# Optimization experiments

Hardware: AMD Instinct MI355X
Metric: run time of the kernel (lower is better)

## Reference

```python
import jax, jax.numpy as jnp
import numpy as np

N = 50000
E = 800000
IN_DIM, HID, LAT, DEC_HID = 256, 256, 128, 512


def _glorot(key, shape):
    fan_in, fan_out = shape
    lim = np.sqrt(6.0 / (fan_in + fan_out))
    return jax.random.uniform(key, shape, jnp.float32, -lim, lim)


def setup_inputs() -> dict:
    key = jax.random.key(0)
    ks = jax.random.split(key, 10)
    x = jax.random.normal(ks[0], (N, IN_DIM), jnp.float32)
    edge_index = jax.random.randint(ks[1], (2, E), 0, N, dtype=jnp.int64)
    return {
        "x": x,
        "edge_index": edge_index,
        "W1": _glorot(ks[2], (IN_DIM, HID)), "b1": jnp.zeros((HID,), jnp.float32),
        "W2": _glorot(ks[3], (HID, LAT)), "b2": jnp.zeros((LAT,), jnp.float32),
        "Wd1": _glorot(ks[4], (LAT, DEC_HID)), "bd1": jnp.zeros((DEC_HID,), jnp.float32),
        "Wd2": _glorot(ks[5], (DEC_HID, IN_DIM)), "bd2": jnp.zeros((IN_DIM,), jnp.float32),
    }


def _gcn_layer(x, src, dst, W, b, num_nodes):
    # linear transform
    xt = x @ W + b                      # [N, out]
    # scatter-mean aggregation over incoming edges (PyG aggr='mean')
    msg = xt[src]                       # [E, out] gather of source features
    summed = jax.ops.segment_sum(msg, dst, num_segments=num_nodes)
    cnt = jax.ops.segment_sum(jnp.ones((src.shape[0],), xt.dtype), dst,
                              num_segments=num_nodes)
    mean = summed / jnp.maximum(cnt, 1.0)[:, None]   # 0 for isolated nodes
    # relu + residual
    return jax.nn.relu(mean) + xt


def reference(x, edge_index, W1, b1, W2, b2, Wd1, bd1, Wd2, bd2):
    src, dst = edge_index[0], edge_index[1]
    h = _gcn_layer(x, src, dst, W1, b1, x.shape[0])
    z = _gcn_layer(h, src, dst, W2, b2, x.shape[0])
    # decoder MLP
    x_hat = jax.nn.relu(z @ Wd1 + bd1) @ Wd2 + bd2
    return (x_hat, z)
```

## Files before the change

kernel.cpp:

```cpp
#include <hip/hip_runtime.h>
#include <hip/hip_bf16.h>

#define TPB 256

typedef __attribute__((ext_vector_type(8))) short short8;
typedef __attribute__((ext_vector_type(4))) float f32x4;

__device__ __forceinline__ unsigned short f2bf(float f) {
    unsigned int u = __float_as_uint(f);
    u = (u + 0x7FFFu + ((u >> 16) & 1u)) >> 16;
    return (unsigned short)u;
}
__device__ __forceinline__ float bflo(unsigned int u) { return __uint_as_float(u << 16); }
__device__ __forceinline__ float bfhi(unsigned int u) { return __uint_as_float(u & 0xFFFF0000u); }

__device__ __forceinline__ void gload16(const void* g, void* l) {
    __builtin_amdgcn_global_load_lds(
        (const __attribute__((address_space(1))) unsigned int*)g,
        (__attribute__((address_space(3))) unsigned int*)l, 16, 0, 0);
}

__global__ void transpose_convert_all(
    const float* __restrict__ Wa, unsigned short* __restrict__ Ta, int Ka, int Na,
    const float* __restrict__ Wb, unsigned short* __restrict__ Tb, int Kb, int Nb,
    const float* __restrict__ Wc, unsigned short* __restrict__ Tc, int Kc, int Nc_,
    const float* __restrict__ Wd, unsigned short* __restrict__ Td, int Kd, int Nd)
{
    __shared__ float tile[32][33];
    int b = blockIdx.x;
    const float* W; unsigned short* T; int K, Nn;
    const int ta = (Na / 32) * (Ka / 32);
    const int tb = (Nb / 32) * (Kb / 32);
    const int tc = (Nc_ / 32) * (Kc / 32);
    if (b < ta)                { W = Wa; T = Ta; K = Ka; Nn = Na; }
    else if (b < ta + tb)      { b -= ta;           W = Wb; T = Tb; K = Kb; Nn = Nb; }
    else if (b < ta + tb + tc) { b -= ta + tb;      W = Wc; T = Tc; K = Kc; Nn = Nc_; }
    else                       { b -= ta + tb + tc; W = Wd; T = Td; K = Kd; Nn = Nd; }
    const int nx = Nn / 32;
    const int n0 = (b % nx) * 32;
    const int k0 = (b / nx) * 32;
    const int tx = threadIdx.x, ty = threadIdx.y;
#pragma unroll
    for (int i = 0; i < 4; ++i)
        tile[ty + i * 8][tx] = W[(size_t)(k0 + ty + i * 8) * Nn + n0 + tx];
    __syncthreads();
#pragma unroll
    for (int i = 0; i < 4; ++i)
        T[(size_t)(n0 + ty + i * 8) * K + k0 + tx] = f2bf(tile[tx][ty + i * 8]);
}

__device__ __forceinline__ void load_a16f(const float* p, short8& lo, short8& hi) {
    float4 f0 = *reinterpret_cast<const float4*>(p);
    float4 f1 = *reinterpret_cast<const float4*>(p + 4);
    float4 f2 = *reinterpret_cast<const float4*>(p + 8);
    float4 f3 = *reinterpret_cast<const float4*>(p + 12);
    lo[0] = (short)f2bf(f0.x); lo[1] = (short)f2bf(f0.y);
    lo[2] = (short)f2bf(f0.z); lo[3] = (short)f2bf(f0.w);
    lo[4] = (short)f2bf(f1.x); lo[5] = (short)f2bf(f1.y);
    lo[6] = (short)f2bf(f1.z); lo[7] = (short)f2bf(f1.w);
    hi[0] = (short)f2bf(f2.x); hi[1] = (short)f2bf(f2.y);
    hi[2] = (short)f2bf(f2.z); hi[3] = (short)f2bf(f2.w);
    hi[4] = (short)f2bf(f3.x); hi[5] = (short)f2bf(f3.y);
    hi[6] = (short)f2bf(f3.z); hi[7] = (short)f2bf(f3.w);
}

__device__ __forceinline__ void copy_out32(unsigned short* C, const float* Cst, const float* bias,
                                           int rowbase, int bn, int M, int Nc, int t, bool doRelu) {
#pragma unroll
    for (int it = 0; it < 2; ++it) {
        const int idx = it * 2048 + t * 8;
        const int row = idx >> 7, col = idx & 127;
        const int m = rowbase + row;
        if (m >= M) continue;
        float4 v0 = *reinterpret_cast<const float4*>(&Cst[idx]);
        float4 v1 = *reinterpret_cast<const float4*>(&Cst[idx + 4]);
        float4 b0 = *reinterpret_cast<const float4*>(&bias[bn + col]);
        float4 b1 = *reinterpret_cast<const float4*>(&bias[bn + col + 4]);
        float o[8] = {v0.x + b0.x, v0.y + b0.y, v0.z + b0.z, v0.w + b0.w,
                      v1.x + b1.x, v1.y + b1.y, v1.z + b1.z, v1.w + b1.w};
        short8 s;
#pragma unroll
        for (int j = 0; j < 8; ++j) {
            const float vv = doRelu ? fmaxf(o[j], 0.f) : o[j];
            s[j] = (short)f2bf(vv);
        }
        *reinterpret_cast<short8*>(&C[(size_t)m * Nc + bn + col]) = s;
    }
}
__device__ __forceinline__ void copy_out32(float* C, const float* Cst, const float* bias,
                                           int rowbase, int bn, int M, int Nc, int t, bool doRelu) {
#pragma unroll
    for (int it = 0; it < 4; ++it) {
        const int idx = it * 1024 + t * 4;
        const int row = idx >> 7, col = idx & 127;
        const int m = rowbase + row;
        if (m >= M) continue;
        float4 v = *reinterpret_cast<const float4*>(&Cst[idx]);
        float4 b = *reinterpret_cast<const float4*>(&bias[bn + col]);
        v.x += b.x; v.y += b.y; v.z += b.z; v.w += b.w;
        if (doRelu) {
            v.x = fmaxf(v.x, 0.f); v.y = fmaxf(v.y, 0.f);
            v.z = fmaxf(v.z, 0.f); v.w = fmaxf(v.w, 0.f);
        }
        *reinterpret_cast<float4*>(&C[(size_t)m * Nc + bn + col]) = v;
    }
}

template <typename TA, typename TC, int K, bool RELU>
__global__ __launch_bounds__(256) void mfma_gemm4(
    const TA* __restrict__ A, const unsigned short* __restrict__ Bt,
    const float* __restrict__ bias, TC* __restrict__ C, int M, int Nc)
{
    __shared__ unsigned short lds_s[2][12288];
    constexpr bool AF32 = (sizeof(TA) == 4);

    const int t  = threadIdx.x;
    const int l  = t & 63;
    const int w  = t >> 6;
    const int wm = w >> 1, wn = w & 1;
    const int bm = blockIdx.x * 64;
    const int bn = blockIdx.y * 128;

    f32x4 acc[2][4] = {};

    const int r4 = t >> 2;
    const int q4 = t & 3;
    const int gmr = bm + r4;
    short8 sa0, sa1;

    auto loadAregs = [&](int k0) {
        if (gmr < M) load_a16f((const float*)A + (size_t)gmr * K + k0 + q4 * 16, sa0, sa1);
        else { sa0 = (short8)0; sa1 = (short8)0; }
    };
    auto writeAregs = [&](int buf) {
        const int s0 = (2 * q4)     ^ (r4 & 7);
        const int s1 = (2 * q4 + 1) ^ (r4 & 7);
        *reinterpret_cast<short8*>(&lds_s[buf][r4 * 64 + s0 * 8]) = sa0;
        *reinterpret_cast<short8*>(&lds_s[buf][r4 * 64 + s1 * 8]) = sa1;
    };
    auto stageA_lds = [&](int buf, int k0) {
#pragma unroll
        for (int ii = 0; ii < 2; ++ii) {
            const int seg = w + ii * 4;
            const int rr  = seg * 8 + (l >> 3);
            const int ss  = l & 7;
            const int gr  = min(bm + rr, M - 1);
            gload16((const unsigned short*)A + (size_t)gr * K + k0 + ((ss ^ (rr & 7)) * 8),
                    &lds_s[buf][seg * 512]);
        }
    };
    auto stageB = [&](int buf, int k0) {
#pragma unroll
        for (int ii = 0; ii < 4; ++ii) {
            const int seg = w + ii * 4;
            const int rr  = seg * 8 + (l >> 3);
            const int ss  = l & 7;
            gload16(Bt + (size_t)(bn + rr) * K + k0 + ((ss ^ (rr & 7)) * 8),
                    &lds_s[buf][4096 + seg * 512]);
        }
    };

    constexpr int S = K / 64;

    if (AF32) {
        loadAregs(0);
        writeAregs(0);
        if (S > 1) loadAregs(64);
    } else {
        stageA_lds(0, 0);
    }
    stageB(0, 0);
    __syncthreads();

#pragma unroll
    for (int step = 0; step < S; ++step) {
        const int k0  = step * 64;
        const int cur = step & 1;

        if (step + 1 < S) {
            if (AF32) writeAregs(cur ^ 1);
            else      stageA_lds(cur ^ 1, k0 + 64);
            stageB(cur ^ 1, k0 + 64);
        }
        if (AF32 && step + 2 < S) loadAregs(k0 + 128);

#pragma unroll
        for (int kk = 0; kk < 2; ++kk) {
            short8 af[2], bf4[4];
#pragma unroll
            for (int mf = 0; mf < 2; ++mf) {
                const int row  = wm * 32 + mf * 16 + (l & 15);
                const int slot = (kk * 4 + (l >> 4)) ^ (row & 7);
                af[mf] = *reinterpret_cast<const short8*>(&lds_s[cur][row * 64 + slot * 8]);
            }
#pragma unroll
            for (int nf = 0; nf < 4; ++nf) {
                const int row  = wn * 64 + nf * 16 + (l & 15);
                const int slot = (kk * 4 + (l >> 4)) ^ (row & 7);
                bf4[nf] = *reinterpret_cast<const short8*>(&lds_s[cur][4096 + row * 64 + slot * 8]);
            }
#pragma unroll
            for (int mf = 0; mf < 2; ++mf)
#pragma unroll
                for (int nf = 0; nf < 4; ++nf)
                    acc[mf][nf] = __builtin_amdgcn_mfma_f32_16x16x32_bf16(
                        af[mf], bf4[nf], acc[mf][nf], 0, 0, 0);
        }
        __syncthreads();
    }

    float* Cst = reinterpret_cast<float*>(lds_s);
#pragma unroll
    for (int p = 0; p < 2; ++p) {
        if (wm == p) {
#pragma unroll
            for (int mf = 0; mf < 2; ++mf)
#pragma unroll
                for (int nf = 0; nf < 4; ++nf)
#pragma unroll
                    for (int rr = 0; rr < 4; ++rr) {
                        const int row = mf * 16 + (l >> 4) * 4 + rr;
                        const int col = wn * 64 + nf * 16 + (l & 15);
                        Cst[row * 128 + col] = acc[mf][nf][rr];
                    }
        }
        __syncthreads();
        copy_out32(C, Cst, bias, bm + p * 32, bn, M, Nc, t, RELU);
        if (p == 0) __syncthreads();
    }
}

__global__ __launch_bounds__(256) void fused_decoder(
    const unsigned short* __restrict__ Z,
    const unsigned short* __restrict__ Wt1,
    const float* __restrict__ b1v,
    const unsigned short* __restrict__ Wt2,
    const float* __restrict__ b2v,
    float* __restrict__ Xh, int M)
{
    __shared__ unsigned short z_s[4096];
    __shared__ unsigned short hd_s[16384];
    __shared__ unsigned short b_s[16384];

    const int t = threadIdx.x;
    const int l = t & 63;
    const int w = t >> 6;
    const int bm = blockIdx.x * 32;

#pragma unroll
    for (int ii = 0; ii < 2; ++ii) {
        const int seg = w + ii * 4;
        const int r   = seg * 4 + (l >> 4);
        const int sl  = l & 15;
        const int gr  = min(bm + r, M - 1);
        gload16(Z + (size_t)gr * 128 + ((sl ^ (r & 15)) * 8), &z_s[seg * 512]);
    }

    auto stageB = [&](const unsigned short* W, int Krow, int rowbase, int k0) {
#pragma unroll
        for (int ii = 0; ii < 8; ++ii) {
            const int seg = w + ii * 4;
            const int rr  = seg * 8 + (l >> 3);
            const int sl  = l & 7;
            gload16(W + (size_t)(rowbase + rr) * Krow + k0 + ((sl ^ (rr & 7)) * 8),
                    &b_s[seg * 512]);
        }
    };

    f32x4 acc[2][4];

#pragma unroll
    for (int p = 0; p < 4; ++p) {
        const int nc = p >> 1, st = p & 1;
        stageB(Wt1, 128, nc * 256, st * 64);
        __syncthreads();
        if (st == 0) {
#pragma unroll
            for (int mf = 0; mf < 2; ++mf)
#pragma unroll
                for (int nf = 0; nf < 4; ++nf) acc[mf][nf] = (f32x4)(0.f);
        }
#pragma unroll
        for (int kk = 0; kk < 2; ++kk) {
            const int kc  = st * 8 + kk * 4 + (l >> 4);
            const int kc2 = kk * 4 + (l >> 4);
            short8 af[2], bf[4];
#pragma unroll
            for (int mf = 0; mf < 2; ++mf) {
                const int r = mf * 16 + (l & 15);
                af[mf] = *reinterpret_cast<const short8*>(&z_s[r * 128 + ((kc ^ (r & 15)) * 8)]);
            }
#pragma unroll
            for (int nf = 0; nf < 4; ++nf) {
                const int r = w * 64 + nf * 16 + (l & 15);
                bf[nf] = *reinterpret_cast<const short8*>(&b_s[r * 64 + ((kc2 ^ (r & 7)) * 8)]);
            }
#pragma unroll
            for (int mf = 0; mf < 2; ++mf)
#pragma unroll
                for (int nf = 0; nf < 4; ++nf)
                    acc[mf][nf] = __builtin_amdgcn_mfma_f32_16x16x32_bf16(
                        af[mf], bf[nf], acc[mf][nf], 0, 0, 0);
        }
        if (st == 1) {
#pragma unroll
            for (int mf = 0; mf < 2; ++mf)
#pragma unroll
                for (int nf = 0; nf < 4; ++nf) {
                    const int c  = nc * 256 + w * 64 + nf * 16 + (l & 15);
                    const float bv = b1v[c];
#pragma unroll
                    for (int rr = 0; rr < 4; ++rr) {
                        const int r = mf * 16 + (l >> 4) * 4 + rr;
                        const float v = fmaxf(acc[mf][nf][rr] + bv, 0.f);
                        hd_s[r * 512 + (((c >> 3) ^ (r & 7)) * 8) + (c & 7)] = f2bf(v);
                    }
                }
        }
        __syncthreads();
    }

#pragma unroll
    for (int mf = 0; mf < 2; ++mf)
#pragma unroll
        for (int nf = 0; nf < 4; ++nf) acc[mf][nf] = (f32x4)(0.f);

    for (int step = 0; step < 8; ++step) {
        stageB(Wt2, 512, 0, step * 64);
        __syncthreads();
#pragma unroll
        for (int kk = 0; kk < 2; ++kk) {
            const int kc  = step * 8 + kk * 4 + (l >> 4);
            const int kc2 = kk * 4 + (l >> 4);
            short8 af[2], bf[4];
#pragma unroll
            for (int mf = 0; mf < 2; ++mf) {
                const int r = mf * 16 + (l & 15);
                af[mf] = *reinterpret_cast<const short8*>(&hd_s[r * 512 + ((kc ^ (r & 7)) * 8)]);
            }
#pragma unroll
            for (int nf = 0; nf < 4; ++nf) {
                const int r = w * 64 + nf * 16 + (l & 15);
                bf[nf] = *reinterpret_cast<const short8*>(&b_s[r * 64 + ((kc2 ^ (r & 7)) * 8)]);
            }
#pragma unroll
            for (int mf = 0; mf < 2; ++mf)
#pragma unroll
                for (int nf = 0; nf < 4; ++nf)
                    acc[mf][nf] = __builtin_amdgcn_mfma_f32_16x16x32_bf16(
                        af[mf], bf[nf], acc[mf][nf], 0, 0, 0);
        }
        __syncthreads();
    }

    float* Cst = reinterpret_cast<float*>(b_s);
#pragma unroll
    for (int mf = 0; mf < 2; ++mf)
#pragma unroll
        for (int nf = 0; nf < 4; ++nf)
#pragma unroll
            for (int rr = 0; rr < 4; ++rr) {
                const int r = mf * 16 + (l >> 4) * 4 + rr;
                const int c = w * 64 + nf * 16 + (l & 15);
                Cst[r * 256 + c] = acc[mf][nf][rr];
            }
    __syncthreads();
#pragma unroll
    for (int it = 0; it < 8; ++it) {
        const int idx = it * 1024 + t * 4;
        const int r = idx >> 8, c = idx & 255;
        if (bm + r < M) {
            float4 v = *reinterpret_cast<const float4*>(&Cst[idx]);
            float4 b = *reinterpret_cast<const float4*>(&b2v[c]);
            v.x += b.x; v.y += b.y; v.z += b.z; v.w += b.w;
            *reinterpret_cast<float4*>(&Xh[(size_t)(bm + r) * 256 + c]) = v;
        }
    }
}

__global__ void hist_kernel(const int* __restrict__ dst, int* __restrict__ counts,
                            int E, int csz)
{
    const int chunk = blockIdx.x & 7;
    const int blk   = blockIdx.x >> 3;
    const int lo = chunk * csz, hi = lo + csz;
    const int base = (blk * TPB + threadIdx.x) * 4;
    if (base + 3 < E) {
        int4 d4 = *reinterpret_cast<const int4*>(dst + base);
        if (d4.x >= lo && d4.x < hi) atomicAdd(&counts[d4.x], 1);
        if (d4.y >= lo && d4.y < hi) atomicAdd(&counts[d4.y], 1);
        if (d4.z >= lo && d4.z < hi) atomicAdd(&counts[d4.z], 1);
        if (d4.w >= lo && d4.w < hi) atomicAdd(&counts[d4.w], 1);
    } else {
        for (int e = base; e < E; ++e) {
            const int d = dst[e];
            if (d >= lo && d < hi) atomicAdd(&counts[d], 1);
        }
    }
}

__global__ void scan1_kernel(const int* __restrict__ counts,
                             int* __restrict__ local, int* __restrict__ bsum, int N)
{
    __shared__ int sh[TPB];
    const int t = threadIdx.x;
    const int base = blockIdx.x * 1024 + t * 4;
    int v[4];
#pragma unroll
    for (int i = 0; i < 4; ++i) v[i] = (base + i < N) ? counts[base + i] : 0;
    const int s = v[0] + v[1] + v[2] + v[3];
    sh[t] = s;
    __syncthreads();
    for (int d = 1; d < TPB; d <<= 1) {
        int x = (t >= d) ? sh[t - d] : 0;
        __syncthreads();
        sh[t] += x;
        __syncthreads();
    }
    int run = sh[t] - s;
#pragma unroll
    for (int i = 0; i < 4; ++i) {
        if (base + i < N) local[base + i] = run;
        run += v[i];
    }
    if (t == TPB - 1) bsum[blockIdx.x] = sh[TPB - 1];
}

__global__ void scan2_kernel(int* __restrict__ bsum, int nb)
{
    __shared__ int sh[TPB];
    const int t = threadIdx.x;
    const int v = (t < nb) ? bsum[t] : 0;
    sh[t] = v;
    __syncthreads();
    for (int d = 1; d < TPB; d <<= 1) {
        int x = (t >= d) ? sh[t - d] : 0;
        __syncthreads();
        sh[t] += x;
        __syncthreads();
    }
    if (t < nb) bsum[t] = sh[t] - v;
}

__global__ void scan3_kernel(int* __restrict__ offsets, int* __restrict__ cursor,
                             const int* __restrict__ bsum, int N)
{
    const int i = blockIdx.x * TPB + threadIdx.x;
    if (i < N) {
        const int o = offsets[i] + bsum[i >> 10];
        offsets[i] = o;
        cursor[i]  = o;
    }
}

__global__ void build_perm_kernel(const int* __restrict__ src, const int* __restrict__ dst,
                                  int* __restrict__ cursor, int* __restrict__ perm,
                                  int E, int csz)
{
    const int chunk = blockIdx.x & 7;
    const int blk   = blockIdx.x >> 3;
    const int lo = chunk * csz, hi = lo + csz;
    const int base = (blk * TPB + threadIdx.x) * 4;
    if (base + 3 < E) {
        int4 d4 = *reinterpret_cast<const int4*>(dst + base);
        if (d4.x >= lo && d4.x < hi) { int p = atomicAdd(&cursor[d4.x], 1); perm[p] = src[base + 0]; }
        if (d4.y >= lo && d4.y < hi) { int p = atomicAdd(&cursor[d4.y], 1); perm[p] = src[base + 1]; }
        if (d4.z >= lo && d4.z < hi) { int p = atomicAdd(&cursor[d4.z], 1); perm[p] = src[base + 2]; }
        if (d4.w >= lo && d4.w < hi) { int p = atomicAdd(&cursor[d4.w], 1); perm[p] = src[base + 3]; }
    } else {
        for (int e = base; e < E; ++e) {
            const int d = dst[e];
            if (d >= lo && d < hi) { int p = atomicAdd(&cursor[d], 1); perm[p] = src[e]; }
        }
    }
}

template <int F, int CH, bool WRITE_ZF32>
__global__ __launch_bounds__(256) void agg_kernel(
    const uint2* __restrict__ xt,
    const int* __restrict__ offsets, const int* __restrict__ counts,
    const int* __restrict__ perm,
    uint2* __restrict__ out, float* __restrict__ zf32, int N)
{
    constexpr int RU  = F / 4;
    constexpr int L   = RU / CH;
    constexpr int NPB = TPB / L;

    const int chunk = blockIdx.x % CH;
    const int node  = (blockIdx.x / CH) * NPB + threadIdx.x / L;
    const int g     = threadIdx.x % L;
    if (node >= N) return;
    const int col = chunk * L + g;

    const int start = offsets[node];
    const int deg   = counts[node];

    float a0 = 0.f, a1 = 0.f, a2 = 0.f, a3 = 0.f;

    for (int base = 0; base < deg; base += L) {
        const int m = min(L, deg - base);
        const int pidx = perm[start + base + ((g < m) ? g : (m - 1))];
        int j = 0;
        for (; j + 4 <= m; j += 4) {
            const int s0 = __shfl(pidx, j + 0, L);
            const int s1 = __shfl(pidx, j + 1, L);
            const int s2 = __shfl(pidx, j + 2, L);
            const int s3 = __shfl(pidx, j + 3, L);
            const uint2 v0 = xt[(size_t)s0 * RU + col];
            const uint2 v1 = xt[(size_t)s1 * RU + col];
            const uint2 v2 = xt[(size_t)s2 * RU + col];
            const uint2 v3 = xt[(size_t)s3 * RU + col];
            a0 += bflo(v0.x) + bflo(v1.x) + bflo(v2.x) + bflo(v3.x);
            a1 += bfhi(v0.x) + bfhi(v1.x) + bfhi(v2.x) + bfhi(v3.x);
            a2 += bflo(v0.y) + bflo(v1.y) + bflo(v2.y) + bflo(v3.y);
            a3 += bfhi(v0.y) + bfhi(v1.y) + bfhi(v2.y) + bfhi(v3.y);
        }
        for (; j < m; ++j) {
            const int s = __shfl(pidx, j, L);
            const uint2 v = xt[(size_t)s * RU + col];
            a0 += bflo(v.x); a1 += bfhi(v.x);
            a2 += bflo(v.y); a3 += bfhi(v.y);
        }
    }

    const float c = (float)max(deg, 1);
    const uint2 xv = xt[(size_t)node * RU + col];
    const float r0 = fmaxf(a0 / c, 0.f) + bflo(xv.x);
    const float r1 = fmaxf(a1 / c, 0.f) + bfhi(xv.x);
    const float r2 = fmaxf(a2 / c, 0.f) + bflo(xv.y);
    const float r3 = fmaxf(a3 / c, 0.f) + bfhi(xv.y);

    uint2 o;
    o.x = (unsigned int)f2bf(r0) | ((unsigned int)f2bf(r1) << 16);
    o.y = (unsigned int)f2bf(r2) | ((unsigned int)f2bf(r3) << 16);
    out[(size_t)node * RU + col] = o;
    if (WRITE_ZF32) {
        float4 z4 = make_float4(r0, r1, r2, r3);
        *reinterpret_cast<float4*>(&zf32[(size_t)node * F + 4 * col]) = z4;
    }
}

extern "C" void kernel_launch(void* const* d_in, const int* in_sizes, int n_in,
                              void* d_out, int out_size, void* d_ws, size_t ws_size,
                              hipStream_t stream)
{
    const int IN_DIM = 256, HID = 256, LAT = 128, DEC_HID = 512;
    const int N = in_sizes[0] / IN_DIM;
    const int E = in_sizes[1] / 2;

    const float* x   = (const float*)d_in[0];
    const int*   ei  = (const int*)d_in[1];
    const float* W1  = (const float*)d_in[2];
    const float* b1  = (const float*)d_in[3];
    const float* W2  = (const float*)d_in[4];
    const float* b2  = (const float*)d_in[5];
    const float* Wd1 = (const float*)d_in[6];
    const float* bd1 = (const float*)d_in[7];
    const float* Wd2 = (const float*)d_in[8];
    const float* bd2 = (const float*)d_in[9];

    const int* src = ei;
    const int* dst = ei + E;

    unsigned short* xt1  = (unsigned short*)d_ws;
    unsigned short* h    = xt1  + (size_t)N * 256;
    unsigned short* xt2  = h    + (size_t)N * 256;
    unsigned short* zbf  = xt2  + (size_t)N * 128;
    unsigned short* wt1  = zbf  + (size_t)N * 128;
    unsigned short* wt2  = wt1  + 256 * 256;
    unsigned short* wtd1 = wt2  + 128 * 256;
    unsigned short* wtd2 = wtd1 + 512 * 128;
    int* counts  = (int*)(wtd2 + 256 * 512);
    int* offsets = counts + N;
    int* cursor  = offsets + N;
    int* bsum    = cursor + N;
    int* perm    = bsum + 256;

    float* out_xhat = (float*)d_out;
    float* out_z    = out_xhat + (size_t)N * IN_DIM;

    dim3 blk(TPB);
    const int mb64 = (N + 63) / 64;
    const int nscan = (N + 1023) / 1024;
    const int csz = (N + 7) / 8;
    const int egrid8 = ((E + TPB * 4 - 1) / (TPB * 4)) * 8;

    {
        const int tiles = (HID/32)*(IN_DIM/32) + (LAT/32)*(HID/32)
                        + (DEC_HID/32)*(LAT/32) + (IN_DIM/32)*(DEC_HID/32);
        transpose_convert_all<<<tiles, dim3(32, 8), 0, stream>>>(
            W1, wt1, IN_DIM, HID,  W2, wt2, HID, LAT,
            Wd1, wtd1, LAT, DEC_HID,  Wd2, wtd2, DEC_HID, IN_DIM);
    }

    hipMemsetAsync(counts, 0, (size_t)N * 4, stream);
    hist_kernel<<<egrid8, blk, 0, stream>>>(dst, counts, E, csz);
    scan1_kernel<<<nscan, blk, 0, stream>>>(counts, offsets, bsum, N);
    scan2_kernel<<<1, blk, 0, stream>>>(bsum, nscan);
    scan3_kernel<<<(N + TPB - 1) / TPB, blk, 0, stream>>>(offsets, cursor, bsum, N);
    build_perm_kernel<<<egrid8, blk, 0, stream>>>(src, dst, cursor, perm, E, csz);

    mfma_gemm4<float, unsigned short, 256, false><<<dim3(mb64, HID / 128), blk, 0, stream>>>(
        x, wt1, b1, xt1, N, HID);
    {
        const int ngroups = (N + 15) / 16;
        agg_kernel<256, 4, false><<<ngroups * 4, blk, 0, stream>>>(
            (const uint2*)xt1, offsets, counts, perm, (uint2*)h, nullptr, N);
    }

    mfma_gemm4<unsigned short, unsigned short, 256, false><<<dim3(mb64, LAT / 128), blk, 0, stream>>>(
        h, wt2, b2, xt2, N, LAT);
    {
        const int ngroups = (N + 15) / 16;
        agg_kernel<128, 2, true><<<ngroups * 2, blk, 0, stream>>>(
            (const uint2*)xt2, offsets, counts, perm, (uint2*)zbf, out_z, N);
    }

    fused_decoder<<<(N + 31) / 32, blk, 0, stream>>>(
        zbf, wtd1, bd1, wtd2, bd2, out_xhat, N);
}
```

Measured before the change: 268.6 us.

## Double-buffer decoder weight staging and split aggregation into source-range passes

The fused decoder now stages weights in two half-size LDS buffers. The next tile is prefetched while MFMAs run on the current one, which removes one barrier per step, and each wave covers 32 output columns in narrower chunks. The aggregation kernels now make two passes over each node's edge list, each gathering only sources in one half of the node range. This is meant to improve L2 locality of the gathers, but it reads the index list twice, adds a branch per edge, and drops the 4-way unrolled gather loop.

```diff
diff --git a/kernel.cpp b/kernel.cpp
--- a/kernel.cpp
+++ b/kernel.cpp
@@ -240,7 +240,7 @@
 {
     __shared__ unsigned short z_s[4096];
     __shared__ unsigned short hd_s[16384];
-    __shared__ unsigned short b_s[16384];
+    __shared__ unsigned short b_s[2][8192];
 
     const int t = threadIdx.x;
     const int l = t & 63;
@@ -256,49 +256,56 @@
         gload16(Z + (size_t)gr * 128 + ((sl ^ (r & 15)) * 8), &z_s[seg * 512]);
     }
 
-    auto stageB = [&](const unsigned short* W, int Krow, int rowbase, int k0) {
-#pragma unroll
-        for (int ii = 0; ii < 8; ++ii) {
+    auto stageHB = [&](int buf, const unsigned short* W, int Krow, int rowbase, int k0) {
+#pragma unroll
+        for (int ii = 0; ii < 4; ++ii) {
             const int seg = w + ii * 4;
             const int rr  = seg * 8 + (l >> 3);
             const int sl  = l & 7;
             gload16(W + (size_t)(rowbase + rr) * Krow + k0 + ((sl ^ (rr & 7)) * 8),
-                    &b_s[seg * 512]);
+                    &b_s[buf][seg * 512]);
         }
     };
 
-    f32x4 acc[2][4];
-
-#pragma unroll
-    for (int p = 0; p < 4; ++p) {
-        const int nc = p >> 1, st = p & 1;
-        stageB(Wt1, 128, nc * 256, st * 64);
-        __syncthreads();
+    stageHB(0, Wt1, 128, 0, 0);
+    __syncthreads();
+
+    f32x4 acc[2][2];
+    int buf = 0;
+#pragma unroll
+    for (int tt = 0; tt < 8; ++tt) {
+        const int rc = tt >> 1, st = tt & 1;
+        if (tt + 1 < 8) {
+            const int nrc = (tt + 1) >> 1, nst = (tt + 1) & 1;
+            stageHB(buf ^ 1, Wt1, 128, nrc * 128, nst * 64);
+        } else {
+            stageHB(buf ^ 1, Wt2, 512, 0, 0);
+        }
         if (st == 0) {
 #pragma unroll
             for (int mf = 0; mf < 2; ++mf)
 #pragma unroll
-                for (int nf = 0; nf < 4; ++nf) acc[mf][nf] = (f32x4)(0.f);
+                for (int nf = 0; nf < 2; ++nf) acc[mf][nf] = (f32x4)(0.f);
         }
 #pragma unroll
         for (int kk = 0; kk < 2; ++kk) {
-            const int kc  = st * 8 + kk * 4 + (l >> 4);
-            const int kc2 = kk * 4 + (l >> 4);
-            short8 af[2], bf[4];
+            const int kcz = st * 8 + kk * 4 + (l >> 4);
+            const int kcb = kk * 4 + (l >> 4);
+            short8 af[2], bf[2];
 #pragma unroll
             for (int mf = 0; mf < 2; ++mf) {
                 const int r = mf * 16 + (l & 15);
-                af[mf] = *reinterpret_cast<const short8*>(&z_s[r * 128 + ((kc ^ (r & 15)) * 8)]);
+                af[mf] = *reinterpret_cast<const short8*>(&z_s[r * 128 + ((kcz ^ (r & 15)) * 8)]);
             }
 #pragma unroll
-            for (int nf = 0; nf < 4; ++nf) {
-                const int r = w * 64 + nf * 16 + (l & 15);
-                bf[nf] = *reinterpret_cast<const short8*>(&b_s[r * 64 + ((kc2 ^ (r & 7)) * 8)]);
+            for (int nf = 0; nf < 2; ++nf) {
+                const int r = w * 32 + nf * 16 + (l & 15);
+                bf[nf] = *reinterpret_cast<const short8*>(&b_s[buf][r * 64 + ((kcb ^ (r & 7)) * 8)]);
             }
 #pragma unroll
             for (int mf = 0; mf < 2; ++mf)
 #pragma unroll
-                for (int nf = 0; nf < 4; ++nf)
+                for (int nf = 0; nf < 2; ++nf)
                     acc[mf][nf] = __builtin_amdgcn_mfma_f32_16x16x32_bf16(
                         af[mf], bf[nf], acc[mf][nf], 0, 0, 0);
         }
@@ -306,8 +313,8 @@
 #pragma unroll
             for (int mf = 0; mf < 2; ++mf)
 #pragma unroll
-                for (int nf = 0; nf < 4; ++nf) {
-                    const int c  = nc * 256 + w * 64 + nf * 16 + (l & 15);
+                for (int nf = 0; nf < 2; ++nf) {
+                    const int c  = rc * 128 + w * 32 + nf * 16 + (l & 15);
                     const float bv = b1v[c];
 #pragma unroll
                     for (int rr = 0; rr < 4; ++rr) {
@@ -318,52 +325,63 @@
                 }
         }
         __syncthreads();
-    }
-
-#pragma unroll
-    for (int mf = 0; mf < 2; ++mf)
-#pragma unroll
-        for (int nf = 0; nf < 4; ++nf) acc[mf][nf] = (f32x4)(0.f);
-
-    for (int step = 0; step < 8; ++step) {
-        stageB(Wt2, 512, 0, step * 64);
-        __syncthreads();
+        buf ^= 1;
+    }
+
+    f32x4 acc2[2][2][2];
+#pragma unroll
+    for (int r2 = 0; r2 < 2; ++r2)
+#pragma unroll
+        for (int mf = 0; mf < 2; ++mf)
+#pragma unroll
+            for (int nf = 0; nf < 2; ++nf) acc2[r2][mf][nf] = (f32x4)(0.f);
+
+#pragma unroll
+    for (int tt = 0; tt < 16; ++tt) {
+        const int rc2 = tt >> 3, step = tt & 7;
+        if (tt + 1 < 16) {
+            const int nrc = (tt + 1) >> 3, nstep = (tt + 1) & 7;
+            stageHB(buf ^ 1, Wt2, 512, nrc * 128, nstep * 64);
+        }
 #pragma unroll
         for (int kk = 0; kk < 2; ++kk) {
-            const int kc  = step * 8 + kk * 4 + (l >> 4);
-            const int kc2 = kk * 4 + (l >> 4);
-            short8 af[2], bf[4];
+            const int kch = step * 8 + kk * 4 + (l >> 4);
+            const int kcb = kk * 4 + (l >> 4);
+            short8 af[2], bf[2];
 #pragma unroll
             for (int mf = 0; mf < 2; ++mf) {
                 const int r = mf * 16 + (l & 15);
-                af[mf] = *reinterpret_cast<const short8*>(&hd_s[r * 512 + ((kc ^ (r & 7)) * 8)]);
+                af[mf] = *reinterpret_cast<const short8*>(&hd_s[r * 512 + ((kch ^ (r & 7)) * 8)]);
             }
 #pragma unroll
-            for (int nf = 0; nf < 4; ++nf) {
-                const int r = w * 64 + nf * 16 + (l & 15);
-                bf[nf] = *reinterpret_cast<const short8*>(&b_s[r * 64 + ((kc2 ^ (r & 7)) * 8)]);
+            for (int nf = 0; nf < 2; ++nf) {
+                const int r = w * 32 + nf * 16 + (l & 15);
+                bf[nf] = *reinterpret_cast<const short8*>(&b_s[buf][r * 64 + ((kcb ^ (r & 7)) * 8)]);
             }
 #pragma unroll
             for (int mf = 0; mf < 2; ++mf)
 #pragma unroll
-                for (int nf = 0; nf < 4; ++nf)
-                    acc[mf][nf] = __builtin_amdgcn_mfma_f32_16x16x32_bf16(
-                        af[mf], bf[nf], acc[mf][nf], 0, 0, 0);
-        }
-        __syncthreads();
+                for (int nf = 0; nf < 2; ++nf)
+                    acc2[rc2][mf][nf] = __builtin_amdgcn_mfma_f32_16x16x32_bf16(
+                        af[mf], bf[nf], acc2[rc2][mf][nf], 0, 0, 0);
+        }
+        __syncthreads();
+        buf ^= 1;
     }
 
     float* Cst = reinterpret_cast<float*>(b_s);
 #pragma unroll
-    for (int mf = 0; mf < 2; ++mf)
-#pragma unroll
-        for (int nf = 0; nf < 4; ++nf)
-#pragma unroll
-            for (int rr = 0; rr < 4; ++rr) {
-                const int r = mf * 16 + (l >> 4) * 4 + rr;
-                const int c = w * 64 + nf * 16 + (l & 15);
-                Cst[r * 256 + c] = acc[mf][nf][rr];
-            }
+    for (int r2 = 0; r2 < 2; ++r2)
+#pragma unroll
+        for (int mf = 0; mf < 2; ++mf)
+#pragma unroll
+            for (int nf = 0; nf < 2; ++nf)
+#pragma unroll
+                for (int rr = 0; rr < 4; ++rr) {
+                    const int r = mf * 16 + (l >> 4) * 4 + rr;
+                    const int c = r2 * 128 + w * 32 + nf * 16 + (l & 15);
+                    Cst[r * 256 + c] = acc2[r2][mf][nf][rr];
+                }
     __syncthreads();
 #pragma unroll
     for (int it = 0; it < 8; ++it) {
@@ -475,7 +493,7 @@
     }
 }
 
-template <int F, int CH, bool WRITE_ZF32>
+template <int F, int CH, int PASSES, bool WRITE_ZF32>
 __global__ __launch_bounds__(256) void agg_kernel(
     const uint2* __restrict__ xt,
     const int* __restrict__ offsets, const int* __restrict__ counts,
@@ -494,32 +512,25 @@
 
     const int start = offsets[node];
     const int deg   = counts[node];
+    const int span  = (N + PASSES - 1) / PASSES;
 
     float a0 = 0.f, a1 = 0.f, a2 = 0.f, a3 = 0.f;
 
-    for (int base = 0; base < deg; base += L) {
-        const int m = min(L, deg - base);
-        const int pidx = perm[start + base + ((g < m) ? g : (m - 1))];
-        int j = 0;
-        for (; j + 4 <= m; j += 4) {
-            const int s0 = __shfl(pidx, j + 0, L);
-            const int s1 = __shfl(pidx, j + 1, L);
-            const int s2 = __shfl(pidx, j + 2, L);
-            const int s3 = __shfl(pidx, j + 3, L);
-            const uint2 v0 = xt[(size_t)s0 * RU + col];
-            const uint2 v1 = xt[(size_t)s1 * RU + col];
-            const uint2 v2 = xt[(size_t)s2 * RU + col];
-            const uint2 v3 = xt[(size_t)s3 * RU + col];
-            a0 += bflo(v0.x) + bflo(v1.x) + bflo(v2.x) + bflo(v3.x);
-            a1 += bfhi(v0.x) + bfhi(v1.x) + bfhi(v2.x) + bfhi(v3.x);
-            a2 += bflo(v0.y) + bflo(v1.y) + bflo(v2.y) + bflo(v3.y);
-            a3 += bfhi(v0.y) + bfhi(v1.y) + bfhi(v2.y) + bfhi(v3.y);
-        }
-        for (; j < m; ++j) {
-            const int s = __shfl(pidx, j, L);
-            const uint2 v = xt[(size_t)s * RU + col];
-            a0 += bflo(v.x); a1 += bfhi(v.x);
-            a2 += bflo(v.y); a3 += bfhi(v.y);
+#pragma unroll
+    for (int pass = 0; pass < PASSES; ++pass) {
+        const int plo = pass * span;
+        const int phi = plo + span;
+        for (int base = 0; base < deg; base += L) {
+            const int m = min(L, deg - base);
+            const int pidx = perm[start + base + ((g < m) ? g : (m - 1))];
+            for (int j = 0; j < m; ++j) {
+                const int s = __shfl(pidx, j, L);
+                if (PASSES == 1 || (s >= plo && s < phi)) {
+                    const uint2 v = xt[(size_t)s * RU + col];
+                    a0 += bflo(v.x); a1 += bfhi(v.x);
+                    a2 += bflo(v.y); a3 += bfhi(v.y);
+                }
+            }
         }
     }
 
@@ -604,7 +615,7 @@
         x, wt1, b1, xt1, N, HID);
     {
         const int ngroups = (N + 15) / 16;
-        agg_kernel<256, 4, false><<<ngroups * 4, blk, 0, stream>>>(
+        agg_kernel<256, 4, 2, false><<<ngroups * 4, blk, 0, stream>>>(
             (const uint2*)xt1, offsets, counts, perm, (uint2*)h, nullptr, N);
     }
 
@@ -612,7 +623,7 @@
         h, wt2, b2, xt2, N, LAT);
     {
         const int ngroups = (N + 15) / 16;
-        agg_kernel<128, 2, true><<<ngroups * 2, blk, 0, stream>>>(
+        agg_kernel<128, 2, 2, true><<<ngroups * 2, blk, 0, stream>>>(
             (const uint2*)xt2, offsets, counts, perm, (uint2*)zbf, out_z, N);
     }
 
```

New measurement: 376.4 us. +40.2%, slower.
